# Performance work log

Hardware: AMD Instinct MI355X
Metric: run time of the kernel (lower is better)

The kernel has to match this reference:

```python
import jax, jax.numpy as jnp
import numpy as np

P, B, N, M, D_LAT = 4, 32, 2048, 512, 128
BETA = 1e-3
BIG = 1e9  # sentinel for masked-out pairwise distances


def quat_to_rotmat(q):
    # q: (..., 4) quaternion (w, x, y, z), normalized then converted
    q = q / jnp.linalg.norm(q, axis=-1, keepdims=True)
    w, x, y, z = q[..., 0], q[..., 1], q[..., 2], q[..., 3]
    R = jnp.stack([
        1 - 2 * (y * y + z * z), 2 * (x * y - w * z), 2 * (x * z + w * y),
        2 * (x * y + w * z), 1 - 2 * (x * x + z * z), 2 * (y * z - w * x),
        2 * (x * z - w * y), 2 * (y * z + w * x), 1 - 2 * (x * x + y * y),
    ], axis=-1)
    return R.reshape(q.shape[:-1] + (3, 3))


def setup_inputs() -> dict:
    key = jax.random.key(0)
    ks = jax.random.split(key, 8)
    return {
        'ipt': jax.random.normal(ks[0], (B, N, 3), jnp.float32),
        'opt': jax.random.normal(ks[1], (P, B, M, 3), jnp.float32),
        'trans': jax.random.normal(ks[2], (P, B, 3), jnp.float32),
        'rots': jax.random.normal(ks[3], (P, B, 4), jnp.float32),
        'probs': jax.random.uniform(ks[4], (P, B, 1), jnp.float32),
        'idx': jax.random.randint(ks[5], (B, N), 0, P),
        'mu': jax.random.normal(ks[6], (B, D_LAT), jnp.float32),
        'logvar': jax.random.normal(ks[7], (B, D_LAT), jnp.float32),
    }


def _parts_distance(ipt, opt, trans, rots, probs, idx):
    # Masked, fully-batched equivalent of the original python double loop:
    # index_select by (idx==i) + _remove_zero_rows are expressed as boolean
    # masks; empty part/sample combinations are excluded via `valid`.
    chamfer_d = 0.0
    coverage = 0.0
    quality = 0.0
    num = 0.0
    nonzero_x = jnp.any(ipt != 0, axis=-1)  # (B, N)
    for i in range(P):  # fixed small part count, structurally distinct slices
        y = opt[i]                                   # (B, M, 3)
        mask_y = jnp.any(y != 0, axis=-1)            # (B, M) _remove_zero_rows
        mx = (idx == i) & nonzero_x                  # (B, N) part selection
        # transform_to_primitives_centric_system: x_local = R (x - t)
        R = quat_to_rotmat(rots[i])                  # (B, 3, 3)
        x = jnp.einsum('bij,bnj->bni', R, ipt - trans[i][:, None, :])
        # pairwise squared distances, (B, N, M)
        D = jnp.sum((x[:, :, None, :] - y[:, None, :, :]) ** 2, axis=-1)
        nx = jnp.sum(mx, axis=-1)                    # (B,)
        ny = jnp.sum(mask_y, axis=-1)                # (B,)
        # quality: mean over valid x of min distance to valid y
        qual = jnp.sum(jnp.where(mx, jnp.min(jnp.where(mask_y[:, None, :], D, BIG), axis=-1), 0.0), axis=-1) / jnp.maximum(nx, 1)
        # coverage: mean over valid y of min distance to valid x
        cov = jnp.sum(jnp.where(mask_y, jnp.min(jnp.where(mx[:, :, None], D, BIG), axis=-2), 0.0), axis=-1) / jnp.maximum(ny, 1)
        cd = qual + cov                              # symmetric chamfer
        valid = (nx > 0) & (ny > 0)                  # x.size(0)!=0 and y.size(0)!=0
        w = jnp.where(valid, probs[i][:, 0], 0.0)    # prob-weighted sum over batch
        n = jnp.sum(valid).astype(jnp.float32)
        has = (n > 0).astype(jnp.float32)
        inv_n = has / jnp.maximum(n, 1.0)
        chamfer_d = chamfer_d + jnp.sum(w * cd) * inv_n
        coverage = coverage + jnp.sum(w * cov) * inv_n
        quality = quality + jnp.sum(w * qual) * inv_n
        num = num + has
    inv_num = 1.0 / jnp.maximum(num, 1.0)
    return chamfer_d * inv_num, coverage * inv_num, quality * inv_num


def KL(mu, logvar):
    # standard VAE KL: sum over latent, mean over batch
    return -0.5 * jnp.sum(1.0 + logvar - mu ** 2 - jnp.exp(logvar)) / mu.shape[0]


def reference(ipt, opt, trans, rots, probs, idx, mu, logvar):
    cds, covs, quals = _parts_distance(ipt, opt, trans, rots, probs, idx)
    kld = KL(mu, logvar)
    return (cds + BETA * kld, cds, covs, quals, kld)
```

## Files before the change

### kernel.cpp

```cpp
#include <hip/hip_runtime.h>
#include <math.h>

#define PP 4
#define BB 32
#define PB (PP * BB)
#define NN 2048
#define MM 512
#define DLAT 128
#define BETA_C 1e-3f
#define BIGV 1e9f
#define SENT 1e8f
#define THREADS 256
#define NCHUNK 2
#define QCH (NN / NCHUNK)
#define CCH (MM / NCHUNK)

__device__ float g_ws[8 * PB];

__device__ __forceinline__ int wave_compact_slot(bool sel, int* s_cnt, int tid) {
    unsigned long long bal = __ballot(sel);
    int lofs = __popcll(bal & ((1ull << (tid & 63)) - 1ull));
    int base = 0;
    if ((tid & 63) == 0 && bal) base = atomicAdd(s_cnt, __popcll(bal));
    base = __shfl(base, 0);
    return base + lofs;
}

template<int SLOTS>
__device__ __forceinline__ float quality_pass(
    const float* __restrict__ syx, const float* __restrict__ syy, const float* __restrict__ syz,
    const float* __restrict__ sxx, const float* __restrict__ sxy, const float* __restrict__ sxz,
    int nx, int base, int tid)
{
    float px[SLOTS], py[SLOTS], pz[SLOTS], mna[SLOTS], mnb[SLOTS];
    bool act[SLOTS];
#pragma unroll
    for (int s = 0; s < SLOTS; ++s) {
        int k = base + s * THREADS + tid;
        act[s] = (k < nx);
        px[s] = act[s] ? sxx[k] : SENT;
        py[s] = act[s] ? sxy[k] : SENT;
        pz[s] = act[s] ? sxz[k] : SENT;
        mna[s] = BIGV; mnb[s] = BIGV;
    }
#pragma unroll 4
    for (int m = 0; m < MM; m += 4) {
        float4 yx = *reinterpret_cast<const float4*>(syx + m);
        float4 yy = *reinterpret_cast<const float4*>(syy + m);
        float4 yz = *reinterpret_cast<const float4*>(syz + m);
#pragma unroll
        for (int s = 0; s < SLOTS; ++s) {
            float dx0 = px[s] - yx.x, dy0 = py[s] - yy.x, dz0 = pz[s] - yz.x;
            float dx1 = px[s] - yx.y, dy1 = py[s] - yy.y, dz1 = pz[s] - yz.y;
            float dx2 = px[s] - yx.z, dy2 = py[s] - yy.z, dz2 = pz[s] - yz.z;
            float dx3 = px[s] - yx.w, dy3 = py[s] - yy.w, dz3 = pz[s] - yz.w;
            float d0 = dx0 * dx0 + dy0 * dy0 + dz0 * dz0;
            float d1 = dx1 * dx1 + dy1 * dy1 + dz1 * dz1;
            float d2 = dx2 * dx2 + dy2 * dy2 + dz2 * dz2;
            float d3 = dx3 * dx3 + dy3 * dy3 + dz3 * dz3;
            mna[s] = fminf(mna[s], fminf(d0, d1));
            mnb[s] = fminf(mnb[s], fminf(d2, d3));
        }
    }
    float sum = 0.0f;
#pragma unroll
    for (int s = 0; s < SLOTS; ++s)
        if (act[s]) sum += fminf(mna[s], mnb[s]);
    return sum;
}

__global__ __launch_bounds__(THREADS) void parts_kernel(
    const float* __restrict__ ipt,
    const float* __restrict__ opt,
    const float* __restrict__ trans,
    const float* __restrict__ rots,
    const int*   __restrict__ idx)
{
    const int b = blockIdx.x;
    const int i = blockIdx.y;
    const int z = blockIdx.z;
    const int tid = threadIdx.x;

    __shared__ float Rm[12];
    __shared__ int s_nx, s_ny;
    __shared__ __align__(16) float syx[MM], syy[MM], syz[MM];
    __shared__ __align__(16) float sxx[NN], sxy[NN], sxz[NN];
    __shared__ float red[THREADS / 64];

    if (tid == 0) {
        s_nx = 0;
        s_ny = 0;
        const float* q = rots + (i * BB + b) * 4;
        float qw = q[0], qx = q[1], qy = q[2], qz = q[3];
        float inv = 1.0f / sqrtf(qw * qw + qx * qx + qy * qy + qz * qz);
        qw *= inv; qx *= inv; qy *= inv; qz *= inv;
        Rm[0] = 1.0f - 2.0f * (qy * qy + qz * qz);
        Rm[1] = 2.0f * (qx * qy - qw * qz);
        Rm[2] = 2.0f * (qx * qz + qw * qy);
        Rm[3] = 2.0f * (qx * qy + qw * qz);
        Rm[4] = 1.0f - 2.0f * (qx * qx + qz * qz);
        Rm[5] = 2.0f * (qy * qz - qw * qx);
        Rm[6] = 2.0f * (qx * qz - qw * qy);
        Rm[7] = 2.0f * (qy * qz + qw * qx);
        Rm[8] = 1.0f - 2.0f * (qx * qx + qy * qy);
        const float* t = trans + (i * BB + b) * 3;
        Rm[9] = t[0]; Rm[10] = t[1]; Rm[11] = t[2];
    }
    __syncthreads();

    const float R0 = Rm[0], R1 = Rm[1], R2 = Rm[2];
    const float R3 = Rm[3], R4 = Rm[4], R5 = Rm[5];
    const float R6 = Rm[6], R7 = Rm[7], R8 = Rm[8];
    const float t0 = Rm[9], t1 = Rm[10], t2 = Rm[11];
    const size_t optbase = ((size_t)i * BB + b) * MM;
    const int pb = i * BB + b;

    if (z < NCHUNK) {
        for (int m = tid; m < MM; m += THREADS) {
            const float* y = opt + (optbase + m) * 3;
            float yx = y[0], yy = y[1], yz = y[2];
            bool v = (yx != 0.0f) | (yy != 0.0f) | (yz != 0.0f);
            if (!v) { yx = SENT; yy = SENT; yz = SENT; }
            syx[m] = yx; syy[m] = yy; syz[m] = yz;
        }
        const int n0 = z * QCH;
        for (int n = n0 + tid; n < n0 + QCH; n += THREADS) {
            const float* p = ipt + ((size_t)b * NN + n) * 3;
            float px = p[0], py = p[1], pz = p[2];
            bool nz = (px != 0.0f) | (py != 0.0f) | (pz != 0.0f);
            bool sel = nz && (idx[b * NN + n] == i);
            int pos = wave_compact_slot(sel, &s_nx, tid);
            if (sel) {
                px -= t0; py -= t1; pz -= t2;
                sxx[pos] = R0 * px + R1 * py + R2 * pz;
                sxy[pos] = R3 * px + R4 * py + R5 * pz;
                sxz[pos] = R6 * px + R7 * py + R8 * pz;
            }
        }
        __syncthreads();
        const int nxc = s_nx;

        float sum;
        if (nxc <= THREADS) {
            sum = quality_pass<1>(syx, syy, syz, sxx, sxy, sxz, nxc, 0, tid);
        } else if (nxc <= 2 * THREADS) {
            sum = quality_pass<2>(syx, syy, syz, sxx, sxy, sxz, nxc, 0, tid);
        } else {
            sum = quality_pass<2>(syx, syy, syz, sxx, sxy, sxz, nxc, 0, tid);
            for (int k0 = 2 * THREADS; k0 < nxc; k0 += THREADS)
                sum += quality_pass<1>(syx, syy, syz, sxx, sxy, sxz, nxc, k0, tid);
        }

        for (int off = 32; off > 0; off >>= 1) sum += __shfl_down(sum, off);
        if ((tid & 63) == 0) red[tid >> 6] = sum;
        __syncthreads();
        if (tid == 0) {
            float tot = red[0] + red[1] + red[2] + red[3];
            g_ws[(0 + z) * PB + pb] = tot;
            g_ws[(4 + z) * PB + pb] = (float)nxc;
        }
    } else {
        const int c = z - NCHUNK;
        const int m = c * CCH + tid;
        const float* y = opt + (optbase + m) * 3;
        float qx = y[0], qy = y[1], qz = y[2];
        bool v = (qx != 0.0f) | (qy != 0.0f) | (qz != 0.0f);
        if (!v) { qx = SENT; qy = SENT; qz = SENT; }
        unsigned long long bal = __ballot(v);
        if ((tid & 63) == 0) atomicAdd(&s_ny, __popcll(bal));

        for (int n = tid; n < NN; n += THREADS) {
            const float* p = ipt + ((size_t)b * NN + n) * 3;
            float px = p[0], py = p[1], pz = p[2];
            bool nz = (px != 0.0f) | (py != 0.0f) | (pz != 0.0f);
            bool sel = nz && (idx[b * NN + n] == i);
            int pos = wave_compact_slot(sel, &s_nx, tid);
            if (sel) {
                px -= t0; py -= t1; pz -= t2;
                sxx[pos] = R0 * px + R1 * py + R2 * pz;
                sxy[pos] = R3 * px + R4 * py + R5 * pz;
                sxz[pos] = R6 * px + R7 * py + R8 * pz;
            }
        }
        __syncthreads();
        const int nx = s_nx;
        const int ny = s_ny;
        const int nx4 = (nx + 3) & ~3;
        if (tid < nx4 - nx) {
            sxx[nx + tid] = SENT; sxy[nx + tid] = SENT; sxz[nx + tid] = SENT;
        }
        __syncthreads();

        float mna = BIGV, mnb = BIGV;
#pragma unroll 4
        for (int k = 0; k < nx4; k += 4) {
            float4 xx = *reinterpret_cast<const float4*>(sxx + k);
            float4 xy = *reinterpret_cast<const float4*>(sxy + k);
            float4 xz = *reinterpret_cast<const float4*>(sxz + k);
            float dx0 = qx - xx.x, dy0 = qy - xy.x, dz0 = qz - xz.x;
            float dx1 = qx - xx.y, dy1 = qy - xy.y, dz1 = qz - xz.y;
            float dx2 = qx - xx.z, dy2 = qy - xy.z, dz2 = qz - xz.z;
            float dx3 = qx - xx.w, dy3 = qy - xy.w, dz3 = qz - xz.w;
            float d0 = dx0 * dx0 + dy0 * dy0 + dz0 * dz0;
            float d1 = dx1 * dx1 + dy1 * dy1 + dz1 * dz1;
            float d2 = dx2 * dx2 + dy2 * dy2 + dz2 * dz2;
            float d3 = dx3 * dx3 + dy3 * dy3 + dz3 * dz3;
            mna = fminf(mna, fminf(d0, d1));
            mnb = fminf(mnb, fminf(d2, d3));
        }
        float sum = v ? fminf(mna, mnb) : 0.0f;

        for (int off = 32; off > 0; off >>= 1) sum += __shfl_down(sum, off);
        if ((tid & 63) == 0) red[tid >> 6] = sum;
        __syncthreads();
        if (tid == 0) {
            float tot = red[0] + red[1] + red[2] + red[3];
            g_ws[(2 + c) * PB + pb] = tot;
            g_ws[(6 + c) * PB + pb] = (float)ny;
        }
    }
}

__global__ __launch_bounds__(256) void finalize_kernel(
    const float* __restrict__ probs,
    const float* __restrict__ mu,
    const float* __restrict__ logvar,
    float* __restrict__ out)
{
    const int tid = threadIdx.x;
    __shared__ float red[4];
    __shared__ float s_wq[PB], s_wc[PB], s_val[PB];

    float kls = 0.0f;
    for (int t = tid; t < BB * DLAT; t += 256) {
        float m_ = mu[t], lv = logvar[t];
        kls += 1.0f + lv - m_ * m_ - expf(lv);
    }
    for (int off = 32; off > 0; off >>= 1) kls += __shfl_down(kls, off);
    if ((tid & 63) == 0) red[tid >> 6] = kls;

    if (tid < PB) {
        float qs  = g_ws[0 * PB + tid] + g_ws[1 * PB + tid];
        float cs  = g_ws[2 * PB + tid] + g_ws[3 * PB + tid];
        float nxf = g_ws[4 * PB + tid] + g_ws[5 * PB + tid];
        float nyf = g_ws[6 * PB + tid] + g_ws[7 * PB + tid];
        bool valid = (nxf > 0.0f) && (nyf > 0.0f);
        float w = valid ? probs[tid] : 0.0f;
        s_wq[tid] = w * (qs / fmaxf(nxf, 1.0f));
        s_wc[tid] = w * (cs / fmaxf(nyf, 1.0f));
        s_val[tid] = valid ? 1.0f : 0.0f;
    }
    __syncthreads();

    if (tid == 0) {
        float kld = -0.5f * (red[0] + red[1] + red[2] + red[3]) / (float)BB;
        float ch = 0.0f, cov = 0.0f, qu = 0.0f, num = 0.0f;
        for (int i = 0; i < PP; ++i) {
            float sq = 0.0f, sc = 0.0f, n = 0.0f;
            for (int bb = 0; bb < BB; ++bb) {
                sq += s_wq[i * BB + bb];
                sc += s_wc[i * BB + bb];
                n += s_val[i * BB + bb];
            }
            float has = (n > 0.0f) ? 1.0f : 0.0f;
            float invn = has / fmaxf(n, 1.0f);
            qu += sq * invn;
            cov += sc * invn;
            ch += (sq + sc) * invn;
            num += has;
        }
        float invnum = 1.0f / fmaxf(num, 1.0f);
        float cds = ch * invnum;
        out[0] = cds + BETA_C * kld;
        out[1] = cds;
        out[2] = cov * invnum;
        out[3] = qu * invnum;
        out[4] = kld;
    }
}

extern "C" void kernel_launch(void* const* d_in, const int* in_sizes, int n_in,
                              void* d_out, int out_size, void* d_ws, size_t ws_size,
                              hipStream_t stream) {
    const float* ipt    = (const float*)d_in[0];
    const float* opt    = (const float*)d_in[1];
    const float* trans  = (const float*)d_in[2];
    const float* rots   = (const float*)d_in[3];
    const float* probs  = (const float*)d_in[4];
    const int*   idx    = (const int*)d_in[5];
    const float* mu     = (const float*)d_in[6];
    const float* logvar = (const float*)d_in[7];
    float* out = (float*)d_out;
    (void)d_ws; (void)ws_size; (void)in_sizes; (void)n_in; (void)out_size;

    dim3 grid(BB, PP, 2 * NCHUNK);
    parts_kernel<<<grid, THREADS, 0, stream>>>(ipt, opt, trans, rots, idx);
    finalize_kernel<<<1, 256, 0, stream>>>(probs, mu, logvar, out);
}
```

Measured before the change: 98.81 us.

## Split chamfer min-search across waves with 512-thread blocks and register tiling

Blocks grow to 512 threads, and each wave now takes a slice of the target points while holding 4 query points per lane. Partial minima are then merged across waves through shared memory. This applies to both the quality direction (x to y) and the coverage direction (y to x, where the padding now rounds up to a multiple of 32). It is meant to raise parallelism and per-thread reuse of shared-memory loads, at the cost of extra syncs, a cross-wave min reduction, and more shared memory per block. The KL loop in the finalize kernel also switches to float4 loads.

```diff
diff --git a/kernel.cpp b/kernel.cpp
--- a/kernel.cpp
+++ b/kernel.cpp
@@ -10,10 +10,12 @@
 #define BETA_C 1e-3f
 #define BIGV 1e9f
 #define SENT 1e8f
-#define THREADS 256
+#define THREADS 512
+#define NWAVE (THREADS / 64)
 #define NCHUNK 2
 #define QCH (NN / NCHUNK)
 #define CCH (MM / NCHUNK)
+#define XMAX (NN + 32)
 
 __device__ float g_ws[8 * PB];
 
@@ -24,49 +26,6 @@
     if ((tid & 63) == 0 && bal) base = atomicAdd(s_cnt, __popcll(bal));
     base = __shfl(base, 0);
     return base + lofs;
-}
-
-template<int SLOTS>
-__device__ __forceinline__ float quality_pass(
-    const float* __restrict__ syx, const float* __restrict__ syy, const float* __restrict__ syz,
-    const float* __restrict__ sxx, const float* __restrict__ sxy, const float* __restrict__ sxz,
-    int nx, int base, int tid)
-{
-    float px[SLOTS], py[SLOTS], pz[SLOTS], mna[SLOTS], mnb[SLOTS];
-    bool act[SLOTS];
-#pragma unroll
-    for (int s = 0; s < SLOTS; ++s) {
-        int k = base + s * THREADS + tid;
-        act[s] = (k < nx);
-        px[s] = act[s] ? sxx[k] : SENT;
-        py[s] = act[s] ? sxy[k] : SENT;
-        pz[s] = act[s] ? sxz[k] : SENT;
-        mna[s] = BIGV; mnb[s] = BIGV;
-    }
-#pragma unroll 4
-    for (int m = 0; m < MM; m += 4) {
-        float4 yx = *reinterpret_cast<const float4*>(syx + m);
-        float4 yy = *reinterpret_cast<const float4*>(syy + m);
-        float4 yz = *reinterpret_cast<const float4*>(syz + m);
-#pragma unroll
-        for (int s = 0; s < SLOTS; ++s) {
-            float dx0 = px[s] - yx.x, dy0 = py[s] - yy.x, dz0 = pz[s] - yz.x;
-            float dx1 = px[s] - yx.y, dy1 = py[s] - yy.y, dz1 = pz[s] - yz.y;
-            float dx2 = px[s] - yx.z, dy2 = py[s] - yy.z, dz2 = pz[s] - yz.z;
-            float dx3 = px[s] - yx.w, dy3 = py[s] - yy.w, dz3 = pz[s] - yz.w;
-            float d0 = dx0 * dx0 + dy0 * dy0 + dz0 * dz0;
-            float d1 = dx1 * dx1 + dy1 * dy1 + dz1 * dz1;
-            float d2 = dx2 * dx2 + dy2 * dy2 + dz2 * dz2;
-            float d3 = dx3 * dx3 + dy3 * dy3 + dz3 * dz3;
-            mna[s] = fminf(mna[s], fminf(d0, d1));
-            mnb[s] = fminf(mnb[s], fminf(d2, d3));
-        }
-    }
-    float sum = 0.0f;
-#pragma unroll
-    for (int s = 0; s < SLOTS; ++s)
-        if (act[s]) sum += fminf(mna[s], mnb[s]);
-    return sum;
 }
 
 __global__ __launch_bounds__(THREADS) void parts_kernel(
@@ -80,12 +39,15 @@
     const int i = blockIdx.y;
     const int z = blockIdx.z;
     const int tid = threadIdx.x;
+    const int lane = tid & 63;
+    const int w = tid >> 6;
 
     __shared__ float Rm[12];
     __shared__ int s_nx, s_ny;
     __shared__ __align__(16) float syx[MM], syy[MM], syz[MM];
-    __shared__ __align__(16) float sxx[NN], sxy[NN], sxz[NN];
-    __shared__ float red[THREADS / 64];
+    __shared__ __align__(16) float sxx[XMAX], sxy[XMAX], sxz[XMAX];
+    __shared__ float pmin[NWAVE][256];
+    __shared__ float red[NWAVE];
 
     if (tid == 0) {
         s_nx = 0;
@@ -115,6 +77,8 @@
     const size_t optbase = ((size_t)i * BB + b) * MM;
     const int pb = i * BB + b;
 
+    float sum = 0.0f;
+
     if (z < NCHUNK) {
         for (int m = tid; m < MM; m += THREADS) {
             const float* y = opt + (optbase + m) * 3;
@@ -139,36 +103,72 @@
         }
         __syncthreads();
         const int nxc = s_nx;
-
-        float sum;
-        if (nxc <= THREADS) {
-            sum = quality_pass<1>(syx, syy, syz, sxx, sxy, sxz, nxc, 0, tid);
-        } else if (nxc <= 2 * THREADS) {
-            sum = quality_pass<2>(syx, syy, syz, sxx, sxy, sxz, nxc, 0, tid);
-        } else {
-            sum = quality_pass<2>(syx, syy, syz, sxx, sxy, sxz, nxc, 0, tid);
-            for (int k0 = 2 * THREADS; k0 < nxc; k0 += THREADS)
-                sum += quality_pass<1>(syx, syy, syz, sxx, sxy, sxz, nxc, k0, tid);
+        const int y0 = w * (MM / NWAVE);
+
+        for (int base = 0; base < nxc; base += 256) {
+            float px[4], py[4], pz[4], mn[4];
+#pragma unroll
+            for (int s = 0; s < 4; ++s) {
+                int k = base + s * 64 + lane;
+                bool a = (k < nxc);
+                px[s] = a ? sxx[k] : SENT;
+                py[s] = a ? sxy[k] : SENT;
+                pz[s] = a ? sxz[k] : SENT;
+                mn[s] = BIGV;
+            }
+#pragma unroll 4
+            for (int j = 0; j < MM / NWAVE; j += 4) {
+                float4 yx = *reinterpret_cast<const float4*>(syx + y0 + j);
+                float4 yy = *reinterpret_cast<const float4*>(syy + y0 + j);
+                float4 yz = *reinterpret_cast<const float4*>(syz + y0 + j);
+#pragma unroll
+                for (int s = 0; s < 4; ++s) {
+                    float dx0 = px[s] - yx.x, dy0 = py[s] - yy.x, dz0 = pz[s] - yz.x;
+                    float dx1 = px[s] - yx.y, dy1 = py[s] - yy.y, dz1 = pz[s] - yz.y;
+                    float dx2 = px[s] - yx.z, dy2 = py[s] - yy.z, dz2 = pz[s] - yz.z;
+                    float dx3 = px[s] - yx.w, dy3 = py[s] - yy.w, dz3 = pz[s] - yz.w;
+                    float d0 = dx0 * dx0 + dy0 * dy0 + dz0 * dz0;
+                    float d1 = dx1 * dx1 + dy1 * dy1 + dz1 * dz1;
+                    float d2 = dx2 * dx2 + dy2 * dy2 + dz2 * dz2;
+                    float d3 = dx3 * dx3 + dy3 * dy3 + dz3 * dz3;
+                    mn[s] = fminf(mn[s], fminf(fminf(d0, d1), fminf(d2, d3)));
+                }
+            }
+#pragma unroll
+            for (int s = 0; s < 4; ++s) pmin[w][s * 64 + lane] = mn[s];
+            __syncthreads();
+            if (tid < 256) {
+                int j = tid;
+                if (base + j < nxc) {
+                    float m = pmin[0][j];
+#pragma unroll
+                    for (int ww = 1; ww < NWAVE; ++ww) m = fminf(m, pmin[ww][j]);
+                    sum += m;
+                }
+            }
+            __syncthreads();
         }
 
         for (int off = 32; off > 0; off >>= 1) sum += __shfl_down(sum, off);
-        if ((tid & 63) == 0) red[tid >> 6] = sum;
+        if (lane == 0) red[w] = sum;
         __syncthreads();
         if (tid == 0) {
-            float tot = red[0] + red[1] + red[2] + red[3];
+            float tot = 0.0f;
+            for (int ww = 0; ww < NWAVE; ++ww) tot += red[ww];
             g_ws[(0 + z) * PB + pb] = tot;
-            g_ws[(4 + z) * PB + pb] = (float)nxc;
+            g_ws[(4 + z) * PB + pb] = (float)s_nx;
         }
     } else {
         const int c = z - NCHUNK;
-        const int m = c * CCH + tid;
-        const float* y = opt + (optbase + m) * 3;
-        float qx = y[0], qy = y[1], qz = y[2];
-        bool v = (qx != 0.0f) | (qy != 0.0f) | (qz != 0.0f);
-        if (!v) { qx = SENT; qy = SENT; qz = SENT; }
-        unsigned long long bal = __ballot(v);
-        if ((tid & 63) == 0) atomicAdd(&s_ny, __popcll(bal));
-
+        if (tid < CCH) {
+            const float* y = opt + (optbase + c * CCH + tid) * 3;
+            float yx = y[0], yy = y[1], yz = y[2];
+            bool v = (yx != 0.0f) | (yy != 0.0f) | (yz != 0.0f);
+            if (!v) { yx = SENT; yy = SENT; yz = SENT; }
+            syx[tid] = yx; syy[tid] = yy; syz[tid] = yz;
+            unsigned long long bal = __ballot(v);
+            if (lane == 0) atomicAdd(&s_ny, __popcll(bal));
+        }
         for (int n = tid; n < NN; n += THREADS) {
             const float* p = ipt + ((size_t)b * NN + n) * 3;
             float px = p[0], py = p[1], pz = p[2];
@@ -185,36 +185,59 @@
         __syncthreads();
         const int nx = s_nx;
         const int ny = s_ny;
-        const int nx4 = (nx + 3) & ~3;
-        if (tid < nx4 - nx) {
+        const int nx32 = (nx + 31) & ~31;
+        if (tid < nx32 - nx) {
             sxx[nx + tid] = SENT; sxy[nx + tid] = SENT; sxz[nx + tid] = SENT;
         }
         __syncthreads();
 
-        float mna = BIGV, mnb = BIGV;
+        float qx[4], qy[4], qz[4], mn[4];
+#pragma unroll
+        for (int s = 0; s < 4; ++s) {
+            int j = s * 64 + lane;
+            qx[s] = syx[j]; qy[s] = syy[j]; qz[s] = syz[j];
+            mn[s] = BIGV;
+        }
+        const int q = nx32 / NWAVE;
+        const int x0 = w * q;
 #pragma unroll 4
-        for (int k = 0; k < nx4; k += 4) {
-            float4 xx = *reinterpret_cast<const float4*>(sxx + k);
-            float4 xy = *reinterpret_cast<const float4*>(sxy + k);
-            float4 xz = *reinterpret_cast<const float4*>(sxz + k);
-            float dx0 = qx - xx.x, dy0 = qy - xy.x, dz0 = qz - xz.x;
-            float dx1 = qx - xx.y, dy1 = qy - xy.y, dz1 = qz - xz.y;
-            float dx2 = qx - xx.z, dy2 = qy - xy.z, dz2 = qz - xz.z;
-            float dx3 = qx - xx.w, dy3 = qy - xy.w, dz3 = qz - xz.w;
-            float d0 = dx0 * dx0 + dy0 * dy0 + dz0 * dz0;
-            float d1 = dx1 * dx1 + dy1 * dy1 + dz1 * dz1;
-            float d2 = dx2 * dx2 + dy2 * dy2 + dz2 * dz2;
-            float d3 = dx3 * dx3 + dy3 * dy3 + dz3 * dz3;
-            mna = fminf(mna, fminf(d0, d1));
-            mnb = fminf(mnb, fminf(d2, d3));
-        }
-        float sum = v ? fminf(mna, mnb) : 0.0f;
+        for (int k = 0; k < q; k += 4) {
+            float4 xx = *reinterpret_cast<const float4*>(sxx + x0 + k);
+            float4 xy = *reinterpret_cast<const float4*>(sxy + x0 + k);
+            float4 xz = *reinterpret_cast<const float4*>(sxz + x0 + k);
+#pragma unroll
+            for (int s = 0; s < 4; ++s) {
+                float dx0 = qx[s] - xx.x, dy0 = qy[s] - xy.x, dz0 = qz[s] - xz.x;
+                float dx1 = qx[s] - xx.y, dy1 = qy[s] - xy.y, dz1 = qz[s] - xz.y;
+                float dx2 = qx[s] - xx.z, dy2 = qy[s] - xy.z, dz2 = qz[s] - xz.z;
+                float dx3 = qx[s] - xx.w, dy3 = qy[s] - xy.w, dz3 = qz[s] - xz.w;
+                float d0 = dx0 * dx0 + dy0 * dy0 + dz0 * dz0;
+                float d1 = dx1 * dx1 + dy1 * dy1 + dz1 * dz1;
+                float d2 = dx2 * dx2 + dy2 * dy2 + dz2 * dz2;
+                float d3 = dx3 * dx3 + dy3 * dy3 + dz3 * dz3;
+                mn[s] = fminf(mn[s], fminf(fminf(d0, d1), fminf(d2, d3)));
+            }
+        }
+#pragma unroll
+        for (int s = 0; s < 4; ++s) pmin[w][s * 64 + lane] = mn[s];
+        __syncthreads();
+        if (tid < CCH) {
+            int j = tid;
+            if (syx[j] != SENT) {
+                float m = pmin[0][j];
+#pragma unroll
+                for (int ww = 1; ww < NWAVE; ++ww) m = fminf(m, pmin[ww][j]);
+                sum += m;
+            }
+        }
+        __syncthreads();
 
         for (int off = 32; off > 0; off >>= 1) sum += __shfl_down(sum, off);
-        if ((tid & 63) == 0) red[tid >> 6] = sum;
+        if (lane == 0) red[w] = sum;
         __syncthreads();
         if (tid == 0) {
-            float tot = red[0] + red[1] + red[2] + red[3];
+            float tot = 0.0f;
+            for (int ww = 0; ww < NWAVE; ++ww) tot += red[ww];
             g_ws[(2 + c) * PB + pb] = tot;
             g_ws[(6 + c) * PB + pb] = (float)ny;
         }
@@ -231,10 +254,15 @@
     __shared__ float red[4];
     __shared__ float s_wq[PB], s_wc[PB], s_val[PB];
 
+    const float4* mu4 = reinterpret_cast<const float4*>(mu);
+    const float4* lv4 = reinterpret_cast<const float4*>(logvar);
     float kls = 0.0f;
-    for (int t = tid; t < BB * DLAT; t += 256) {
-        float m_ = mu[t], lv = logvar[t];
-        kls += 1.0f + lv - m_ * m_ - expf(lv);
+    for (int t = tid; t < BB * DLAT / 4; t += 256) {
+        float4 m4 = mu4[t], l4 = lv4[t];
+        kls += (1.0f + l4.x - m4.x * m4.x - expf(l4.x))
+             + (1.0f + l4.y - m4.y * m4.y - expf(l4.y))
+             + (1.0f + l4.z - m4.z * m4.z - expf(l4.z))
+             + (1.0f + l4.w - m4.w * m4.w - expf(l4.w));
     }
     for (int off = 32; off > 0; off >>= 1) kls += __shfl_down(kls, off);
     if ((tid & 63) == 0) red[tid >> 6] = kls;
```

After: 95.23 us. 3.6% less time.
